# Kernel optimization log

Hardware: AMD Instinct MI355X
Metric: run time of the kernel (lower is better)

## Reference

```python
import jax, jax.numpy as jnp
import numpy as np

# dims: B batch, T timesteps, V nodes, D in-features, C channels, d pos-emb dim,
# TS = t_size (spatio-temporal window), P prediction steps, L layers (=4, fixed by GLU(C*4))
B, T, V, D, C, d, TS, P, L = 4, 12, 512, 1, 64, 8, 3, 12, 4
BETA = TS - 1


def setup_inputs() -> dict:
    key = jax.random.key(0)
    ks = jax.random.split(key, 30)
    n = lambda i, shape, s=1.0: jax.random.normal(ks[i], shape, dtype=jnp.float32) * s
    return dict(
        x=n(0, (B, T, V, D)),
        sape=n(1, (V, d)),
        tape=n(2, (B, T, 1, d)),
        srpe=n(3, (V, V, d)),
        trpe=n(4, (TS, 1, d)),
        zeros_x=jnp.zeros((B, BETA, V, C), jnp.float32),
        zeros_tape=jnp.zeros((B, BETA, 1, d), jnp.float32),
        range_mask=(jax.random.uniform(ks[5], (B, V, TS * V)) < 0.5).astype(jnp.float32),
        Wi=n(6, (D, C), D ** -0.5), bi=n(7, (C,), 0.02),
        gc_mu=n(8, (L, 6, d)), gc_sig=n(9, (L, 6, d), 0.5),
        Wg=n(10, (L, C, 2 * C), C ** -0.5), bg=n(11, (L, 2 * C), 0.02),
        Wsp=n(12, (L, d, 2 * C), d ** -0.5), Wtp=n(13, (L, d, 2 * C), d ** -0.5),
        fs_w=n(14, (L, C, C, T), (C * T) ** -0.5), fs_b=n(15, (L, C), 0.02),
        glu1_w=n(16, (L, 2 * C, C), C ** -0.5), glu1_b=n(17, (L, 2 * C), 0.02),
        gout_w=n(18, (8 * C, 4 * C), (4 * C) ** -0.5), gout_b=n(19, (8 * C,), 0.02),
        out_w=n(20, (P, 4 * C), (4 * C) ** -0.5), out_b=n(21, (P,), 0.02),
    )


def _glu_cv(w, b, y):
    # 1x1-conv GLU over channel dim of y: (B, Cin, V) -> (B, Cin, V)
    z = jnp.einsum('oc,bcv->bov', w, y) + b[None, :, None]
    zl, zr = jnp.split(z, 2, axis=1)
    return zl * jax.nn.sigmoid(zr)


def _forward(x, sape, tape, srpe, trpe, Wi, bi, gc_mu, gc_sig, Wg, bg, Wsp, Wtp,
             fs_w, fs_b, glu1_w, glu1_b, gout_w, gout_b, out_w, out_b,
             zeros_x, zeros_tape, range_mask):
    b_, t_ = x.shape[0], x.shape[1]
    v_ = sape.shape[0]
    ts = trpe.shape[0]
    widx = jnp.arange(t_)[:, None] + jnp.arange(ts)  # (T, t_size) sliding-window indices
    h = x @ Wi + bi                                   # InputLayer: B,T,V,C
    tape_pad = jnp.concatenate([zeros_tape, tape], axis=1)  # B,T+beta,1,d
    skips = []
    for l in range(gc_mu.shape[0]):
        mu, sig = gc_mu[l], gc_sig[l]
        gc = lambda emb, i: jnp.sum(-0.5 * (emb - mu[i]) ** 2 * sig[i] ** 2, axis=-1)
        # STPRI: Gaussian position-aware relation inference
        base = gc(sape, 0)[:, None] + gc(sape, 1)[None, :] + gc(srpe, 4)        # (V_i, V_j)
        per_t = gc(tape, 2)[:, :, 0][:, :, None] \
              + gc(tape_pad, 3)[:, :, 0][:, widx] \
              + gc(trpe, 5)[:, 0]                                               # B,T,t_size
        S = jnp.exp(per_t[:, :, :, None, None] + base)                          # B,T,k,i,j (<=1, safe)
        S = S.transpose(0, 1, 4, 2, 3).reshape(b_, t_, v_, ts * v_)             # B,T,j,(k*V+i)
        S = S * range_mask[:, None]                                             # masked relations
        # STPGConv: masked graph conv over the t_size*V window + gating
        x_pad = jnp.concatenate([zeros_x, h], axis=1)                           # B,T+beta,V,C
        xw = x_pad[:, widx].reshape(b_, t_, ts * v_, -1)                        # B,T,t_size*V,C
        g = jnp.einsum('btjm,btmc->btjc', S, xw) @ Wg[l] + bg[l]                # B,T,V,2C
        g = g + sape @ Wsp[l] + tape @ Wtp[l]                                   # +SE(V,2C) +TE(B,T,1,2C)
        gl, gr = jnp.split(g, 2, axis=-1)
        h = gl * jax.nn.sigmoid(gr)                                             # B,T,V,C
        # GFS: conv over time (kernel (1,T)) + GLU -> B,C,V
        y = jnp.einsum('bcvt,oct->bov', h.transpose(0, 3, 2, 1), fs_w[l]) + fs_b[l][None, :, None]
        skips.append(_glu_cv(glu1_w[l], glu1_b[l], y))
    s = _glu_cv(gout_w, gout_b, jnp.concatenate(skips, axis=1))                  # B,4C,V
    return jnp.einsum('oc,bcv->bov', out_w, s) + out_b[None, :, None]            # B,P,V


def reference(x, sape, tape, srpe, trpe, zeros_x, zeros_tape, range_mask, Wi, bi,
              gc_mu, gc_sig, Wg, bg, Wsp, Wtp, fs_w, fs_b, glu1_w, glu1_b,
              gout_w, gout_b, out_w, out_b):
    return _forward(x, sape, tape, srpe, trpe, Wi, bi, gc_mu, gc_sig, Wg, bg, Wsp, Wtp,
                    fs_w, fs_b, glu1_w, glu1_b, gout_w, gout_b, out_w, out_b,
                    zeros_x, zeros_tape, range_mask)
```

## Files before the change

kernel.cpp:

```cpp
#include <hip/hip_runtime.h>
#include <math.h>


typedef unsigned short u16;
typedef __attribute__((ext_vector_type(8))) short short8;
typedef __attribute__((ext_vector_type(4))) float f32x4;
typedef __attribute__((ext_vector_type(8))) unsigned short u16x8;
typedef __attribute__((ext_vector_type(4))) unsigned short u16x4;

#define MFMA16(a, b, c) __builtin_amdgcn_mfma_f32_16x16x32_bf16((a), (b), (c), 0, 0, 0)

__device__ __forceinline__ float b2f(u16 u) {
  union { unsigned int i; float f; } x; x.i = ((unsigned int)u) << 16; return x.f;
}
__device__ __forceinline__ u16 f2b(float f) {
  union { float f; unsigned int i; } x; x.f = f;
  unsigned int r = x.i + 0x7FFFu + ((x.i >> 16) & 1u);
  return (u16)(r >> 16);
}
__device__ __forceinline__ void ld8f(const float* __restrict__ p, float* f) {
  f32x4 a = *(const f32x4*)p;
  f32x4 b = *(const f32x4*)(p + 4);
  #pragma unroll
  for (int i = 0; i < 4; ++i) { f[i] = a[i]; f[4 + i] = b[i]; }
}
__device__ __forceinline__ float gcf(const float* e, const float* __restrict__ mu,
                                     const float* __restrict__ sg) {
  float s = 0.f;
  #pragma unroll
  for (int i = 0; i < 8; ++i) {
    float dm = e[i] - mu[i];
    s += dm * dm * sg[i] * sg[i];
  }
  return -0.5f * s;
}
__device__ __forceinline__ float sigm(float v) { return 1.0f / (1.0f + expf(-v)); }

__global__ __launch_bounds__(256) void prep_kernel(
    const float* __restrict__ x, const float* __restrict__ sape,
    const float* __restrict__ tape, const float* __restrict__ srpe,
    const float* __restrict__ trpe, const float* __restrict__ Wi,
    const float* __restrict__ bi, const float* __restrict__ gmu,
    const float* __restrict__ gsg, const float* __restrict__ Wg,
    const float* __restrict__ bg, const float* __restrict__ Wsp,
    const float* __restrict__ Wtp, const float* __restrict__ fsw,
    const float* __restrict__ mask,
    const float* __restrict__ g1w, const float* __restrict__ gw,
    const float* __restrict__ ow,
    u16* __restrict__ hT0, u16* __restrict__ Abf,
    float* __restrict__ spb, float* __restrict__ tpb,
    u16* __restrict__ fswT, u16* __restrict__ WgT, float* __restrict__ ev,
    u16* __restrict__ g1wB, u16* __restrict__ gwB, u16* __restrict__ owB) {
  const int tid = threadIdx.x;
  int bid = blockIdx.x;

  if (bid < 768) {
    int gid = bid * 256 + tid;
    int i8 = gid & 63, c = (gid >> 6) & 63, bt = gid >> 12;
    float xv[8];
    ld8f(&x[bt * 512 + i8 * 8], xv);
    float wic = Wi[c], bic = bi[c];
    u16x8 hv;
    #pragma unroll
    for (int ii = 0; ii < 8; ++ii) hv[ii] = f2b(xv[ii] * wic + bic);
    *(u16x8*)&hT0[gid * 8] = hv;
    return;
  }
  bid -= 768;
  if (bid < 1024) {
    int gid = bid * 256 + tid;
    int i = gid & 511, j = gid >> 9;
    float fi[8], fj[8], fr[8];
    ld8f(sape + i * 8, fi);
    ld8f(sape + j * 8, fj);
    ld8f(srpe + ((size_t)i * 512 + j) * 8, fr);
    u16 eb[4];
    #pragma unroll
    for (int l = 0; l < 4; ++l) {
      const float* mub = gmu + l * 48;
      const float* sgb = gsg + l * 48;
      float s = gcf(fi, mub + 0, sgb + 0)
              + gcf(fj, mub + 8, sgb + 8)
              + gcf(fr, mub + 32, sgb + 32);
      eb[l] = f2b(expf(s));
    }
    #pragma unroll
    for (int b = 0; b < 4; ++b)
      #pragma unroll
      for (int k = 0; k < 3; ++k) {
        float mv = mask[((size_t)(b * 512 + j)) * 1536 + k * 512 + i];
        u16 m = (mv != 0.f) ? (u16)0xFFFFu : (u16)0;
        #pragma unroll
        for (int l = 0; l < 4; ++l)
          Abf[((size_t)((l * 4 + b) * 512 + j)) * 1536 + k * 512 + i] = eb[l] & m;
      }
    return;
  }
  bid -= 1024;
  if (bid < 1024) {
    int gid = bid * 256 + tid;
    int o = gid & 127, j = (gid >> 7) & 511, l = gid >> 16;
    float a = 0.f;
    #pragma unroll
    for (int dd = 0; dd < 8; ++dd)
      a += sape[j * 8 + dd] * Wsp[(l * 8 + dd) * 128 + o];
    spb[gid] = a;
    return;
  }
  bid -= 1024;
  if (bid < 96) {
    int gid = bid * 256 + tid;
    int o = gid & 127, bt = (gid >> 7) % 48, l = gid / 6144;
    float a = bg[l * 128 + o];
    #pragma unroll
    for (int dd = 0; dd < 8; ++dd)
      a += tape[bt * 8 + dd] * Wtp[(l * 8 + dd) * 128 + o];
    tpb[gid] = a;
    return;
  }
  bid -= 96;
  if (bid < 768) {
    int gid = bid * 256 + tid;
    int kidx = gid % 768, rest = gid / 768;
    int o = rest & 63, l = rest >> 6;
    int c = kidx & 63, tt = kidx >> 6;
    fswT[gid] = f2b(fsw[((l * 64 + o) * 64 + c) * 12 + tt]);
    return;
  }
  bid -= 768;
  if (bid < 128) {
    int gid = bid * 256 + tid;
    int c = gid & 63, o = (gid >> 6) & 127, l = gid >> 13;
    WgT[gid] = f2b(Wg[(l * 64 + c) * 128 + o]);
    return;
  }
  bid -= 128;
  if (bid < 3) {
    int gid = bid * 256 + tid;
    if (gid < 576) {
      int k = gid % 3, t = (gid / 3) % 12, b = (gid / 36) % 4, l = gid / 144;
      const float* mub = gmu + l * 48;
      const float* sgb = gsg + l * 48;
      float e2[8], e3[8], e5[8];
      ld8f(tape + (b * 12 + t) * 8, e2);
      int tp = t + k - 2;
      if (tp >= 0) ld8f(tape + (b * 12 + tp) * 8, e3);
      else {
        #pragma unroll
        for (int ii = 0; ii < 8; ++ii) e3[ii] = 0.f;
      }
      ld8f(trpe + k * 8, e5);
      float s = gcf(e2, mub + 16, sgb + 16)
              + gcf(e3, mub + 24, sgb + 24)
              + gcf(e5, mub + 40, sgb + 40);
      ev[gid] = expf(s);
    }
    return;
  }
  bid -= 3;
  if (bid < 128) {
    int gid = bid * 256 + tid;
    g1wB[gid] = f2b(g1w[gid]);
    return;
  }
  bid -= 128;
  if (bid < 512) {
    int gid = bid * 256 + tid;
    gwB[gid] = f2b(gw[gid]);
    return;
  }
  bid -= 512;
  {
    int gid = bid * 256 + tid;
    if (gid < 3072) owB[gid] = f2b(ow[gid]);
  }
}

__global__ __launch_bounds__(256) void agg_kernel(
    const u16* __restrict__ Abfl, const u16* __restrict__ hT,
    u16* __restrict__ G) {
  __shared__ u16 As[128][72];
  __shared__ u16 Bs[128][72];
  const int tid = threadIdx.x, wid = tid >> 6, lane = tid & 63;
  const int l16 = lane & 15, quad = lane >> 4;
  const int bid = blockIdx.x;
  const int nt = bid % 6;
  const int mt = (bid / 6) & 3;
  const int k  = (bid / 24) % 3;
  const int b  = bid / 72;
  const int wm = wid >> 1, wn = wid & 1;

  const u16* Arow0 = Abfl + ((size_t)(b * 512 + mt * 128)) * 1536 + k * 512;
  f32x4 acc[4][4] = {};

  for (int it = 0; it < 8; ++it) {
    const int i0 = it * 64;
    #pragma unroll
    for (int s = 0; s < 4; ++s) {
      int idx = s * 256 + tid;
      int r = idx >> 3, ch = (idx & 7) * 8;
      *(u16x8*)&As[r][ch] = *(const u16x8*)&Arow0[(size_t)r * 1536 + i0 + ch];
      int tp = nt * 2 + (r >> 6), c = r & 63;
      *(u16x8*)&Bs[r][ch] =
          *(const u16x8*)&hT[((size_t)((b * 12 + tp) * 64 + c)) * 512 + i0 + ch];
    }
    __syncthreads();
    #pragma unroll
    for (int ks = 0; ks < 2; ++ks) {
      short8 af[4], bf[4];
      #pragma unroll
      for (int mb = 0; mb < 4; ++mb)
        af[mb] = *(const short8*)&As[wm * 64 + mb * 16 + l16][ks * 32 + quad * 8];
      #pragma unroll
      for (int nb = 0; nb < 4; ++nb)
        bf[nb] = *(const short8*)&Bs[wn * 64 + nb * 16 + l16][ks * 32 + quad * 8];
      #pragma unroll
      for (int mb = 0; mb < 4; ++mb)
        #pragma unroll
        for (int nb = 0; nb < 4; ++nb)
          acc[mb][nb] = MFMA16(af[mb], bf[nb], acc[mb][nb]);
    }
    __syncthreads();
  }

  u16* base = &As[0][0];
  #pragma unroll
  for (int mb = 0; mb < 4; ++mb)
    #pragma unroll
    for (int nb = 0; nb < 4; ++nb) {
      int n = wn * 64 + nb * 16 + l16;
      #pragma unroll
      for (int r = 0; r < 4; ++r) {
        int m = wm * 64 + mb * 16 + quad * 4 + r;
        base[m * 128 + n] = f2b(acc[mb][nb][r]);
      }
    }
  __syncthreads();
  u16* Gp = G + ((size_t)((b * 3 + k) * 512 + mt * 128)) * 768 + nt * 128;
  #pragma unroll
  for (int s = 0; s < 8; ++s) {
    int idx = s * 256 + tid;
    int m = idx >> 4, ch = (idx & 15) * 8;
    *(u16x8*)&Gp[(size_t)m * 768 + ch] = *(const u16x8*)&base[m * 128 + ch];
  }
}

__global__ __launch_bounds__(256) void combine_kernel(
    const u16* __restrict__ G, const float* __restrict__ evl,
    const u16* __restrict__ WgTl, const float* __restrict__ spbl,
    const float* __restrict__ tpbl, const u16* __restrict__ fswTl,
    u16* __restrict__ hTout, float* __restrict__ yptl) {
  __shared__ u16 aggL[128][72];
  __shared__ u16 hL[128][72];
  const int tid = threadIdx.x, wid = tid >> 6, lane = tid & 63;
  const int l16 = lane & 15, quad = lane >> 4;
  const int bid = blockIdx.x;
  const int mt = bid & 3;
  const int bt = bid >> 2;
  const int b = bt / 12, t = bt - b * 12;

  {
    int j = tid >> 1;
    int c0 = (tid & 1) * 32;
    float accv[32];
    #pragma unroll
    for (int ii = 0; ii < 32; ++ii) accv[ii] = 0.f;
    #pragma unroll
    for (int k = 0; k < 3; ++k) {
      int tp = t + k - 2;
      if (tp < 0) continue;
      float ek = evl[bt * 3 + k];
      const u16* gp = &G[((size_t)((b * 3 + k) * 512 + mt * 128 + j)) * 768 + tp * 64 + c0];
      #pragma unroll
      for (int s = 0; s < 4; ++s) {
        u16x8 gv = *(const u16x8*)&gp[s * 8];
        #pragma unroll
        for (int ii = 0; ii < 8; ++ii) accv[s * 8 + ii] += b2f(gv[ii]) * ek;
      }
    }
    #pragma unroll
    for (int s = 0; s < 4; ++s) {
      u16x8 ov;
      #pragma unroll
      for (int ii = 0; ii < 8; ++ii) ov[ii] = f2b(accv[s * 8 + ii]);
      *(u16x8*)&aggL[j][c0 + s * 8] = ov;
    }
  }
  __syncthreads();

  f32x4 acc2[8][2] = {};
  #pragma unroll
  for (int ks = 0; ks < 2; ++ks) {
    short8 bf[2];
    #pragma unroll
    for (int nb = 0; nb < 2; ++nb)
      bf[nb] = *(const short8*)&aggL[wid * 32 + nb * 16 + l16][ks * 32 + quad * 8];
    #pragma unroll
    for (int mb = 0; mb < 8; ++mb) {
      short8 a = *(const short8*)&WgTl[(mb * 16 + l16) * 64 + ks * 32 + quad * 8];
      acc2[mb][0] = MFMA16(a, bf[0], acc2[mb][0]);
      acc2[mb][1] = MFMA16(a, bf[1], acc2[mb][1]);
    }
  }

  #pragma unroll
  for (int mb = 0; mb < 4; ++mb) {
    int ob = mb * 16 + quad * 4;
    #pragma unroll
    for (int nb = 0; nb < 2; ++nb) {
      int jl = wid * 32 + nb * 16 + l16;
      int jg = mt * 128 + jl;
      f32x4 spl = *(const f32x4*)&spbl[jg * 128 + ob];
      f32x4 spr = *(const f32x4*)&spbl[jg * 128 + 64 + ob];
      f32x4 tpl = *(const f32x4*)&tpbl[bt * 128 + ob];
      f32x4 tpr = *(const f32x4*)&tpbl[bt * 128 + 64 + ob];
      #pragma unroll
      for (int r = 0; r < 4; ++r) {
        float vl = acc2[mb][nb][r] + spl[r] + tpl[r];
        float vr = acc2[mb + 4][nb][r] + spr[r] + tpr[r];
        u16 hb = f2b(vl * sigm(vr));
        hTout[((size_t)((b * 12 + t) * 64 + ob + r)) * 512 + jg] = hb;
        hL[jl][ob + r] = hb;
      }
    }
  }
  __syncthreads();

  f32x4 accY[4][2] = {};
  #pragma unroll
  for (int ks = 0; ks < 2; ++ks) {
    short8 bfv[2];
    #pragma unroll
    for (int nb = 0; nb < 2; ++nb)
      bfv[nb] = *(const short8*)&hL[wid * 32 + nb * 16 + l16][ks * 32 + quad * 8];
    #pragma unroll
    for (int mb = 0; mb < 4; ++mb) {
      short8 a = *(const short8*)&fswTl[(mb * 16 + l16) * 768 + t * 64 + ks * 32 + quad * 8];
      accY[mb][0] = MFMA16(a, bfv[0], accY[mb][0]);
      accY[mb][1] = MFMA16(a, bfv[1], accY[mb][1]);
    }
  }
  #pragma unroll
  for (int mb = 0; mb < 4; ++mb)
    #pragma unroll
    for (int nb = 0; nb < 2; ++nb) {
      int j = mt * 128 + wid * 32 + nb * 16 + l16;
      #pragma unroll
      for (int r = 0; r < 4; ++r) {
        int o = mb * 16 + quad * 4 + r;
        yptl[((size_t)(bt * 64 + o)) * 512 + j] = accY[mb][nb][r];
      }
    }
}

__global__ __launch_bounds__(256) void reduce_kernel(
    const float* __restrict__ ypt, const float* __restrict__ fsb,
    u16* __restrict__ yB) {
  int gid = blockIdx.x * 256 + threadIdx.x;
  int j4 = gid & 127, o = (gid >> 7) & 63, b = (gid >> 13) & 3, l = gid >> 15;
  const float* base = &ypt[(size_t)l * 1572864 +
                           ((size_t)((b * 12) * 64 + o)) * 512 + j4 * 4];
  float fb = fsb[l * 64 + o];
  f32x4 s = {fb, fb, fb, fb};
  #pragma unroll
  for (int t = 0; t < 12; ++t) s += *(const f32x4*)&base[(size_t)t * 32768];
  u16x4 pk;
  #pragma unroll
  for (int ii = 0; ii < 4; ++ii) pk[ii] = f2b(s[ii]);
  *(u16x4*)&yB[((size_t)((l * 4 + b) * 64 + o)) * 512 + j4 * 4] = pk;
}

__global__ __launch_bounds__(256) void glu1cat_kernel(
    const u16* __restrict__ yB, const u16* __restrict__ g1wB,
    const float* __restrict__ g1b, u16* __restrict__ catB) {
  __shared__ u16 yL[128][72];
  const int tid = threadIdx.x, wid = tid >> 6, lane = tid & 63;
  const int l16 = lane & 15, quad = lane >> 4;
  const int l = blockIdx.x >> 4;
  const int b = (blockIdx.x >> 2) & 3;
  const int v0 = (blockIdx.x & 3) * 128;

  {
    int o = tid & 63, sv = tid >> 6;
    const u16* src = &yB[((size_t)((l * 4 + b) * 64 + o)) * 512 + v0 + sv * 32];
    u16x8 p0 = *(const u16x8*)&src[0];
    u16x8 p1 = *(const u16x8*)&src[8];
    u16x8 p2 = *(const u16x8*)&src[16];
    u16x8 p3 = *(const u16x8*)&src[24];
    #pragma unroll
    for (int ii = 0; ii < 8; ++ii) {
      yL[sv * 32 + ii][o] = p0[ii];
      yL[sv * 32 + 8 + ii][o] = p1[ii];
      yL[sv * 32 + 16 + ii][o] = p2[ii];
      yL[sv * 32 + 24 + ii][o] = p3[ii];
    }
  }
  __syncthreads();

  f32x4 acc[2][8] = {};
  #pragma unroll
  for (int ks = 0; ks < 2; ++ks) {
    short8 a0 = *(const short8*)&g1wB[l * 8192 + (wid * 16 + l16) * 64 +
                                      ks * 32 + quad * 8];
    short8 a1 = *(const short8*)&g1wB[l * 8192 + (64 + wid * 16 + l16) * 64 +
                                      ks * 32 + quad * 8];
    #pragma unroll
    for (int nb = 0; nb < 8; ++nb) {
      short8 bf = *(const short8*)&yL[nb * 16 + l16][ks * 32 + quad * 8];
      acc[0][nb] = MFMA16(a0, bf, acc[0][nb]);
      acc[1][nb] = MFMA16(a1, bf, acc[1][nb]);
    }
  }
  #pragma unroll
  for (int nb = 0; nb < 8; ++nb) {
    int v = v0 + nb * 16 + l16;
    int oc = wid * 16 + quad * 4;
    u16x4 pk;
    #pragma unroll
    for (int r = 0; r < 4; ++r) {
      float zl = acc[0][nb][r] + g1b[l * 128 + oc + r];
      float zr = acc[1][nb][r] + g1b[l * 128 + 64 + oc + r];
      pk[r] = f2b(zl * sigm(zr));
    }
    *(u16x4*)&catB[((size_t)(b * 512 + v)) * 256 + l * 64 + oc] = pk;
  }
}

__global__ __launch_bounds__(256) void gout_kernel(
    const u16* __restrict__ catB, const u16* __restrict__ gwB,
    const float* __restrict__ gb, u16* __restrict__ sB) {
  __shared__ u16 cL[64][264];
  const int tid = threadIdx.x, wid = tid >> 6, lane = tid & 63;
  const int l16 = lane & 15, quad = lane >> 4;
  const int wm = wid >> 1, wn = wid & 1;
  const int b = blockIdx.x >> 6;
  const int v0 = ((blockIdx.x >> 3) & 7) * 64;
  const int cc0 = (blockIdx.x & 7) * 32;

  {
    int v = tid >> 2, seg = (tid & 3) * 64;
    const u16* src = &catB[((size_t)(b * 512 + v0 + v)) * 256 + seg];
    #pragma unroll
    for (int s = 0; s < 8; ++s)
      *(u16x8*)&cL[v][seg + s * 8] = *(const u16x8*)&src[s * 8];
  }
  __syncthreads();

  f32x4 acc[2][2] = {};
  #pragma unroll
  for (int ks = 0; ks < 8; ++ks) {
    short8 aL = *(const short8*)&gwB[(cc0 + wm * 16 + l16) * 256 +
                                     ks * 32 + quad * 8];
    short8 aH = *(const short8*)&gwB[(256 + cc0 + wm * 16 + l16) * 256 +
                                     ks * 32 + quad * 8];
    #pragma unroll
    for (int nb = 0; nb < 2; ++nb) {
      short8 bf = *(const short8*)&cL[wn * 32 + nb * 16 + l16][ks * 32 + quad * 8];
      acc[0][nb] = MFMA16(aL, bf, acc[0][nb]);
      acc[1][nb] = MFMA16(aH, bf, acc[1][nb]);
    }
  }
  #pragma unroll
  for (int nb = 0; nb < 2; ++nb) {
    int v = v0 + wn * 32 + nb * 16 + l16;
    int cc = cc0 + wm * 16 + quad * 4;
    u16x4 pk;
    #pragma unroll
    for (int r = 0; r < 4; ++r) {
      float zl = acc[0][nb][r] + gb[cc + r];
      float zr = acc[1][nb][r] + gb[256 + cc + r];
      pk[r] = f2b(zl * sigm(zr));
    }
    *(u16x4*)&sB[((size_t)(b * 512 + v)) * 256 + cc] = pk;
  }
}

__global__ __launch_bounds__(256) void head_kernel(
    const u16* __restrict__ sB, const u16* __restrict__ owB,
    const float* __restrict__ obv, float* __restrict__ out) {
  const int tid = threadIdx.x, wid = tid >> 6, lane = tid & 63;
  const int l16 = lane & 15, quad = lane >> 4;
  const int b = blockIdx.x >> 3;
  const int v0 = (blockIdx.x & 7) * 64;

  f32x4 acc = {};
  #pragma unroll
  for (int ks = 0; ks < 8; ++ks) {
    short8 a;
    if (l16 < 12) a = *(const short8*)&owB[l16 * 256 + ks * 32 + quad * 8];
    else {
      #pragma unroll
      for (int ii = 0; ii < 8; ++ii) a[ii] = 0;
    }
    short8 bf = *(const short8*)&sB[((size_t)(b * 512 + v0 + wid * 16 + l16)) * 256 +
                                    ks * 32 + quad * 8];
    acc = MFMA16(a, bf, acc);
  }
  #pragma unroll
  for (int r = 0; r < 4; ++r) {
    int p = quad * 4 + r;
    if (p < 12)
      out[(b * 12 + p) * 512 + v0 + wid * 16 + l16] = acc[r] + obv[p];
  }
}

extern "C" void kernel_launch(void* const* d_in, const int* in_sizes, int n_in,
                              void* d_out, int out_size, void* d_ws, size_t ws_size,
                              hipStream_t stream) {
  const float* x    = (const float*)d_in[0];
  const float* sape = (const float*)d_in[1];
  const float* tape = (const float*)d_in[2];
  const float* srpe = (const float*)d_in[3];
  const float* trpe = (const float*)d_in[4];
  const float* mask = (const float*)d_in[7];
  const float* Wi   = (const float*)d_in[8];
  const float* bi   = (const float*)d_in[9];
  const float* gmu  = (const float*)d_in[10];
  const float* gsg  = (const float*)d_in[11];
  const float* Wg   = (const float*)d_in[12];
  const float* bg   = (const float*)d_in[13];
  const float* Wsp  = (const float*)d_in[14];
  const float* Wtp  = (const float*)d_in[15];
  const float* fsw  = (const float*)d_in[16];
  const float* fsb  = (const float*)d_in[17];
  const float* g1w  = (const float*)d_in[18];
  const float* g1b  = (const float*)d_in[19];
  const float* gow  = (const float*)d_in[20];
  const float* gob  = (const float*)d_in[21];
  const float* ow   = (const float*)d_in[22];
  const float* obv  = (const float*)d_in[23];

  char* w = (char*)d_ws;
  u16*   hT_a = (u16*)(w + 0);
  u16*   hT_b = (u16*)(w + 3145728);
  u16*   Abf  = (u16*)(w + 6291456);
  u16*   G    = (u16*)(w + 31457280);
  u16*   fswT = (u16*)(w + 40894464);
  u16*   WgT  = (u16*)(w + 41287680);
  u16*   g1wB = (u16*)(w + 41353216);
  u16*   gwB  = (u16*)(w + 41418752);
  u16*   owB  = (u16*)(w + 41680896);
  float* spb  = (float*)(w + 41689088);
  float* tpb  = (float*)(w + 42737664);
  float* ev   = (float*)(w + 42835968);
  float* ypt  = (float*)(w + 42852352);
  u16*   yB   = (u16*)(w + 68018176);
  u16*   catB = (u16*)(w + 70115328);
  u16*   sB   = (u16*)(w + 71163904);

  prep_kernel<<<4463, 256, 0, stream>>>(x, sape, tape, srpe, trpe, Wi, bi, gmu, gsg,
                                        Wg, bg, Wsp, Wtp, fsw, mask, g1w, gow, ow,
                                        hT_a, Abf, spb, tpb, fswT, WgT, ev,
                                        g1wB, gwB, owB);
  u16* hin = hT_a;
  u16* hout = hT_b;
  for (int l = 0; l < 4; ++l) {
    agg_kernel<<<288, 256, 0, stream>>>(Abf + (size_t)l * 3145728, hin, G);
    combine_kernel<<<192, 256, 0, stream>>>(G, ev + l * 144, WgT + l * 8192,
                                            spb + l * 65536, tpb + l * 6144,
                                            fswT + l * 49152, hout,
                                            ypt + (size_t)l * 1572864);
    u16* tmp = hin; hin = hout; hout = tmp;
  }
  reduce_kernel<<<512, 256, 0, stream>>>(ypt, fsb, yB);
  glu1cat_kernel<<<64, 256, 0, stream>>>(yB, g1wB, g1b, catB);
  gout_kernel<<<256, 256, 0, stream>>>(catB, gwB, gob, sB);
  head_kernel<<<32, 256, 0, stream>>>(sB, owB, obv, (float*)d_out);
}
```

Before: 247.6 us.

## Fuse all stages into one persistent kernel with grid-wide barriers

Replaces the sequence of thirteen kernel launches with a single persistent kernel of 256 blocks. Each block loops over the original block indices of every stage, and stages are separated by software grid barriers built from atomic counters. This removes launch overhead and the inter-kernel gaps. In exchange it adds barrier spin cost, needs a memset of the counters each call, and relies on all 256 blocks being co-resident. Stages with more than 256 jobs, such as prep and agg, now run in multiple waves.

```diff
diff --git a/kernel.cpp b/kernel.cpp
--- a/kernel.cpp
+++ b/kernel.cpp
@@ -36,34 +36,39 @@
 }
 __device__ __forceinline__ float sigm(float v) { return 1.0f / (1.0f + expf(-v)); }
 
-__global__ __launch_bounds__(256) void prep_kernel(
-    const float* __restrict__ x, const float* __restrict__ sape,
-    const float* __restrict__ tape, const float* __restrict__ srpe,
-    const float* __restrict__ trpe, const float* __restrict__ Wi,
-    const float* __restrict__ bi, const float* __restrict__ gmu,
-    const float* __restrict__ gsg, const float* __restrict__ Wg,
-    const float* __restrict__ bg, const float* __restrict__ Wsp,
-    const float* __restrict__ Wtp, const float* __restrict__ fsw,
-    const float* __restrict__ mask,
-    const float* __restrict__ g1w, const float* __restrict__ gw,
-    const float* __restrict__ ow,
-    u16* __restrict__ hT0, u16* __restrict__ Abf,
-    float* __restrict__ spb, float* __restrict__ tpb,
-    u16* __restrict__ fswT, u16* __restrict__ WgT, float* __restrict__ ev,
-    u16* __restrict__ g1wB, u16* __restrict__ gwB, u16* __restrict__ owB) {
+__device__ __forceinline__ void gsync(int* bar) {
+  __syncthreads();
+  if (threadIdx.x == 0) {
+    __threadfence();
+    atomicAdd(bar, 1);
+    while (atomicAdd(bar, 0) < 256) __builtin_amdgcn_s_sleep(8);
+    __threadfence();
+  }
+  __syncthreads();
+}
+
+struct MegaArgs {
+  const float *x, *sape, *tape, *srpe, *trpe, *Wi, *bi, *gmu, *gsg, *Wg, *bg,
+              *Wsp, *Wtp, *fsw, *mask, *g1w, *gw, *ow, *fsb, *g1b, *gob, *obv;
+  u16 *hT_a, *hT_b, *Abf, *G, *fswT, *WgT, *g1wB, *gwB, *owB, *yB, *catB, *sB;
+  float *spb, *tpb, *ev, *ypt;
+  float *outp;
+  int *bars;
+};
+
+__device__ void prep_body(const MegaArgs& a, int bid) {
   const int tid = threadIdx.x;
-  int bid = blockIdx.x;
 
   if (bid < 768) {
     int gid = bid * 256 + tid;
     int i8 = gid & 63, c = (gid >> 6) & 63, bt = gid >> 12;
     float xv[8];
-    ld8f(&x[bt * 512 + i8 * 8], xv);
-    float wic = Wi[c], bic = bi[c];
+    ld8f(&a.x[bt * 512 + i8 * 8], xv);
+    float wic = a.Wi[c], bic = a.bi[c];
     u16x8 hv;
     #pragma unroll
     for (int ii = 0; ii < 8; ++ii) hv[ii] = f2b(xv[ii] * wic + bic);
-    *(u16x8*)&hT0[gid * 8] = hv;
+    *(u16x8*)&a.hT_a[gid * 8] = hv;
     return;
   }
   bid -= 768;
@@ -71,14 +76,14 @@
     int gid = bid * 256 + tid;
     int i = gid & 511, j = gid >> 9;
     float fi[8], fj[8], fr[8];
-    ld8f(sape + i * 8, fi);
-    ld8f(sape + j * 8, fj);
-    ld8f(srpe + ((size_t)i * 512 + j) * 8, fr);
+    ld8f(a.sape + i * 8, fi);
+    ld8f(a.sape + j * 8, fj);
+    ld8f(a.srpe + ((size_t)i * 512 + j) * 8, fr);
     u16 eb[4];
     #pragma unroll
     for (int l = 0; l < 4; ++l) {
-      const float* mub = gmu + l * 48;
-      const float* sgb = gsg + l * 48;
+      const float* mub = a.gmu + l * 48;
+      const float* sgb = a.gsg + l * 48;
       float s = gcf(fi, mub + 0, sgb + 0)
               + gcf(fj, mub + 8, sgb + 8)
               + gcf(fr, mub + 32, sgb + 32);
@@ -88,11 +93,11 @@
     for (int b = 0; b < 4; ++b)
       #pragma unroll
       for (int k = 0; k < 3; ++k) {
-        float mv = mask[((size_t)(b * 512 + j)) * 1536 + k * 512 + i];
+        float mv = a.mask[((size_t)(b * 512 + j)) * 1536 + k * 512 + i];
         u16 m = (mv != 0.f) ? (u16)0xFFFFu : (u16)0;
         #pragma unroll
         for (int l = 0; l < 4; ++l)
-          Abf[((size_t)((l * 4 + b) * 512 + j)) * 1536 + k * 512 + i] = eb[l] & m;
+          a.Abf[((size_t)((l * 4 + b) * 512 + j)) * 1536 + k * 512 + i] = eb[l] & m;
       }
     return;
   }
@@ -100,22 +105,22 @@
   if (bid < 1024) {
     int gid = bid * 256 + tid;
     int o = gid & 127, j = (gid >> 7) & 511, l = gid >> 16;
-    float a = 0.f;
+    float s = 0.f;
     #pragma unroll
     for (int dd = 0; dd < 8; ++dd)
-      a += sape[j * 8 + dd] * Wsp[(l * 8 + dd) * 128 + o];
-    spb[gid] = a;
+      s += a.sape[j * 8 + dd] * a.Wsp[(l * 8 + dd) * 128 + o];
+    a.spb[gid] = s;
     return;
   }
   bid -= 1024;
   if (bid < 96) {
     int gid = bid * 256 + tid;
     int o = gid & 127, bt = (gid >> 7) % 48, l = gid / 6144;
-    float a = bg[l * 128 + o];
+    float s = a.bg[l * 128 + o];
     #pragma unroll
     for (int dd = 0; dd < 8; ++dd)
-      a += tape[bt * 8 + dd] * Wtp[(l * 8 + dd) * 128 + o];
-    tpb[gid] = a;
+      s += a.tape[bt * 8 + dd] * a.Wtp[(l * 8 + dd) * 128 + o];
+    a.tpb[gid] = s;
     return;
   }
   bid -= 96;
@@ -124,14 +129,14 @@
     int kidx = gid % 768, rest = gid / 768;
     int o = rest & 63, l = rest >> 6;
     int c = kidx & 63, tt = kidx >> 6;
-    fswT[gid] = f2b(fsw[((l * 64 + o) * 64 + c) * 12 + tt]);
+    a.fswT[gid] = f2b(a.fsw[((l * 64 + o) * 64 + c) * 12 + tt]);
     return;
   }
   bid -= 768;
   if (bid < 128) {
     int gid = bid * 256 + tid;
     int c = gid & 63, o = (gid >> 6) & 127, l = gid >> 13;
-    WgT[gid] = f2b(Wg[(l * 64 + c) * 128 + o]);
+    a.WgT[gid] = f2b(a.Wg[(l * 64 + c) * 128 + o]);
     return;
   }
   bid -= 128;
@@ -139,51 +144,38 @@
     int gid = bid * 256 + tid;
     if (gid < 576) {
       int k = gid % 3, t = (gid / 3) % 12, b = (gid / 36) % 4, l = gid / 144;
-      const float* mub = gmu + l * 48;
-      const float* sgb = gsg + l * 48;
+      const float* mub = a.gmu + l * 48;
+      const float* sgb = a.gsg + l * 48;
       float e2[8], e3[8], e5[8];
-      ld8f(tape + (b * 12 + t) * 8, e2);
+      ld8f(a.tape + (b * 12 + t) * 8, e2);
       int tp = t + k - 2;
-      if (tp >= 0) ld8f(tape + (b * 12 + tp) * 8, e3);
+      if (tp >= 0) ld8f(a.tape + (b * 12 + tp) * 8, e3);
       else {
         #pragma unroll
         for (int ii = 0; ii < 8; ++ii) e3[ii] = 0.f;
       }
-      ld8f(trpe + k * 8, e5);
+      ld8f(a.trpe + k * 8, e5);
       float s = gcf(e2, mub + 16, sgb + 16)
               + gcf(e3, mub + 24, sgb + 24)
               + gcf(e5, mub + 40, sgb + 40);
-      ev[gid] = expf(s);
+      a.ev[gid] = expf(s);
     }
     return;
   }
   bid -= 3;
-  if (bid < 128) {
-    int gid = bid * 256 + tid;
-    g1wB[gid] = f2b(g1w[gid]);
-    return;
-  }
+  if (bid < 128) { int gid = bid * 256 + tid; a.g1wB[gid] = f2b(a.g1w[gid]); return; }
   bid -= 128;
-  if (bid < 512) {
-    int gid = bid * 256 + tid;
-    gwB[gid] = f2b(gw[gid]);
-    return;
-  }
+  if (bid < 512) { int gid = bid * 256 + tid; a.gwB[gid] = f2b(a.gw[gid]); return; }
   bid -= 512;
-  {
-    int gid = bid * 256 + tid;
-    if (gid < 3072) owB[gid] = f2b(ow[gid]);
-  }
-}
-
-__global__ __launch_bounds__(256) void agg_kernel(
-    const u16* __restrict__ Abfl, const u16* __restrict__ hT,
-    u16* __restrict__ G) {
-  __shared__ u16 As[128][72];
-  __shared__ u16 Bs[128][72];
+  { int gid = bid * 256 + tid; if (gid < 3072) a.owB[gid] = f2b(a.ow[gid]); }
+}
+
+__device__ void agg_body(const MegaArgs& a, int bid, const u16* __restrict__ Abfl,
+                         const u16* __restrict__ hT, char* smem) {
+  u16 (*As)[72] = (u16 (*)[72])smem;
+  u16 (*Bs)[72] = (u16 (*)[72])(smem + 18432);
   const int tid = threadIdx.x, wid = tid >> 6, lane = tid & 63;
   const int l16 = lane & 15, quad = lane >> 4;
-  const int bid = blockIdx.x;
   const int nt = bid % 6;
   const int mt = (bid / 6) & 3;
   const int k  = (bid / 24) % 3;
@@ -223,7 +215,7 @@
     __syncthreads();
   }
 
-  u16* base = &As[0][0];
+  u16* base = (u16*)smem;
   #pragma unroll
   for (int mb = 0; mb < 4; ++mb)
     #pragma unroll
@@ -236,25 +228,29 @@
       }
     }
   __syncthreads();
-  u16* Gp = G + ((size_t)((b * 3 + k) * 512 + mt * 128)) * 768 + nt * 128;
+  u16* Gp = a.G + ((size_t)((b * 3 + k) * 512 + mt * 128)) * 768 + nt * 128;
   #pragma unroll
   for (int s = 0; s < 8; ++s) {
     int idx = s * 256 + tid;
     int m = idx >> 4, ch = (idx & 15) * 8;
     *(u16x8*)&Gp[(size_t)m * 768 + ch] = *(const u16x8*)&base[m * 128 + ch];
   }
-}
-
-__global__ __launch_bounds__(256) void combine_kernel(
-    const u16* __restrict__ G, const float* __restrict__ evl,
-    const u16* __restrict__ WgTl, const float* __restrict__ spbl,
-    const float* __restrict__ tpbl, const u16* __restrict__ fswTl,
-    u16* __restrict__ hTout, float* __restrict__ yptl) {
-  __shared__ u16 aggL[128][72];
-  __shared__ u16 hL[128][72];
+  __syncthreads();
+}
+
+__device__ void combine_body(const MegaArgs& a, int bid, int l,
+                             u16* __restrict__ hTout, char* smem) {
+  u16 (*aggL)[72] = (u16 (*)[72])smem;
+  u16 (*hL)[72]   = (u16 (*)[72])(smem + 18432);
+  const float* evl  = a.ev  + l * 144;
+  const u16*   WgTl = a.WgT + l * 8192;
+  const float* spbl = a.spb + l * 65536;
+  const float* tpbl = a.tpb + l * 6144;
+  const u16*   fswTl = a.fswT + l * 49152;
+  float* yptl = a.ypt + (size_t)l * 1572864;
+
   const int tid = threadIdx.x, wid = tid >> 6, lane = tid & 63;
   const int l16 = lane & 15, quad = lane >> 4;
-  const int bid = blockIdx.x;
   const int mt = bid & 3;
   const int bt = bid >> 2;
   const int b = bt / 12, t = bt - b * 12;
@@ -270,7 +266,7 @@
       int tp = t + k - 2;
       if (tp < 0) continue;
       float ek = evl[bt * 3 + k];
-      const u16* gp = &G[((size_t)((b * 3 + k) * 512 + mt * 128 + j)) * 768 + tp * 64 + c0];
+      const u16* gp = &a.G[((size_t)((b * 3 + k) * 512 + mt * 128 + j)) * 768 + tp * 64 + c0];
       #pragma unroll
       for (int s = 0; s < 4; ++s) {
         u16x8 gv = *(const u16x8*)&gp[s * 8];
@@ -297,9 +293,9 @@
       bf[nb] = *(const short8*)&aggL[wid * 32 + nb * 16 + l16][ks * 32 + quad * 8];
     #pragma unroll
     for (int mb = 0; mb < 8; ++mb) {
-      short8 a = *(const short8*)&WgTl[(mb * 16 + l16) * 64 + ks * 32 + quad * 8];
-      acc2[mb][0] = MFMA16(a, bf[0], acc2[mb][0]);
-      acc2[mb][1] = MFMA16(a, bf[1], acc2[mb][1]);
+      short8 aa = *(const short8*)&WgTl[(mb * 16 + l16) * 64 + ks * 32 + quad * 8];
+      acc2[mb][0] = MFMA16(aa, bf[0], acc2[mb][0]);
+      acc2[mb][1] = MFMA16(aa, bf[1], acc2[mb][1]);
     }
   }
 
@@ -335,9 +331,9 @@
       bfv[nb] = *(const short8*)&hL[wid * 32 + nb * 16 + l16][ks * 32 + quad * 8];
     #pragma unroll
     for (int mb = 0; mb < 4; ++mb) {
-      short8 a = *(const short8*)&fswTl[(mb * 16 + l16) * 768 + t * 64 + ks * 32 + quad * 8];
-      accY[mb][0] = MFMA16(a, bfv[0], accY[mb][0]);
-      accY[mb][1] = MFMA16(a, bfv[1], accY[mb][1]);
+      short8 aa = *(const short8*)&fswTl[(mb * 16 + l16) * 768 + t * 64 + ks * 32 + quad * 8];
+      accY[mb][0] = MFMA16(aa, bfv[0], accY[mb][0]);
+      accY[mb][1] = MFMA16(aa, bfv[1], accY[mb][1]);
     }
   }
   #pragma unroll
@@ -351,38 +347,35 @@
         yptl[((size_t)(bt * 64 + o)) * 512 + j] = accY[mb][nb][r];
       }
     }
-}
-
-__global__ __launch_bounds__(256) void reduce_kernel(
-    const float* __restrict__ ypt, const float* __restrict__ fsb,
-    u16* __restrict__ yB) {
-  int gid = blockIdx.x * 256 + threadIdx.x;
+  __syncthreads();
+}
+
+__device__ void reduce_body(const MegaArgs& a, int bid) {
+  int gid = bid * 256 + threadIdx.x;
   int j4 = gid & 127, o = (gid >> 7) & 63, b = (gid >> 13) & 3, l = gid >> 15;
-  const float* base = &ypt[(size_t)l * 1572864 +
-                           ((size_t)((b * 12) * 64 + o)) * 512 + j4 * 4];
-  float fb = fsb[l * 64 + o];
+  const float* base = &a.ypt[(size_t)l * 1572864 +
+                             ((size_t)((b * 12) * 64 + o)) * 512 + j4 * 4];
+  float fb = a.fsb[l * 64 + o];
   f32x4 s = {fb, fb, fb, fb};
   #pragma unroll
   for (int t = 0; t < 12; ++t) s += *(const f32x4*)&base[(size_t)t * 32768];
   u16x4 pk;
   #pragma unroll
   for (int ii = 0; ii < 4; ++ii) pk[ii] = f2b(s[ii]);
-  *(u16x4*)&yB[((size_t)((l * 4 + b) * 64 + o)) * 512 + j4 * 4] = pk;
-}
-
-__global__ __launch_bounds__(256) void glu1cat_kernel(
-    const u16* __restrict__ yB, const u16* __restrict__ g1wB,
-    const float* __restrict__ g1b, u16* __restrict__ catB) {
-  __shared__ u16 yL[128][72];
+  *(u16x4*)&a.yB[((size_t)((l * 4 + b) * 64 + o)) * 512 + j4 * 4] = pk;
+}
+
+__device__ void glu1cat_body(const MegaArgs& a, int bid, char* smem) {
+  u16 (*yL)[72] = (u16 (*)[72])smem;
   const int tid = threadIdx.x, wid = tid >> 6, lane = tid & 63;
   const int l16 = lane & 15, quad = lane >> 4;
-  const int l = blockIdx.x >> 4;
-  const int b = (blockIdx.x >> 2) & 3;
-  const int v0 = (blockIdx.x & 3) * 128;
+  const int l = bid >> 4;
+  const int b = (bid >> 2) & 3;
+  const int v0 = (bid & 3) * 128;
 
   {
     int o = tid & 63, sv = tid >> 6;
-    const u16* src = &yB[((size_t)((l * 4 + b) * 64 + o)) * 512 + v0 + sv * 32];
+    const u16* src = &a.yB[((size_t)((l * 4 + b) * 64 + o)) * 512 + v0 + sv * 32];
     u16x8 p0 = *(const u16x8*)&src[0];
     u16x8 p1 = *(const u16x8*)&src[8];
     u16x8 p2 = *(const u16x8*)&src[16];
@@ -400,10 +393,10 @@
   f32x4 acc[2][8] = {};
   #pragma unroll
   for (int ks = 0; ks < 2; ++ks) {
-    short8 a0 = *(const short8*)&g1wB[l * 8192 + (wid * 16 + l16) * 64 +
-                                      ks * 32 + quad * 8];
-    short8 a1 = *(const short8*)&g1wB[l * 8192 + (64 + wid * 16 + l16) * 64 +
-                                      ks * 32 + quad * 8];
+    short8 a0 = *(const short8*)&a.g1wB[l * 8192 + (wid * 16 + l16) * 64 +
+                                        ks * 32 + quad * 8];
+    short8 a1 = *(const short8*)&a.g1wB[l * 8192 + (64 + wid * 16 + l16) * 64 +
+                                        ks * 32 + quad * 8];
     #pragma unroll
     for (int nb = 0; nb < 8; ++nb) {
       short8 bf = *(const short8*)&yL[nb * 16 + l16][ks * 32 + quad * 8];
@@ -418,28 +411,27 @@
     u16x4 pk;
     #pragma unroll
     for (int r = 0; r < 4; ++r) {
-      float zl = acc[0][nb][r] + g1b[l * 128 + oc + r];
-      float zr = acc[1][nb][r] + g1b[l * 128 + 64 + oc + r];
+      float zl = acc[0][nb][r] + a.g1b[l * 128 + oc + r];
+      float zr = acc[1][nb][r] + a.g1b[l * 128 + 64 + oc + r];
       pk[r] = f2b(zl * sigm(zr));
     }
-    *(u16x4*)&catB[((size_t)(b * 512 + v)) * 256 + l * 64 + oc] = pk;
-  }
-}
-
-__global__ __launch_bounds__(256) void gout_kernel(
-    const u16* __restrict__ catB, const u16* __restrict__ gwB,
-    const float* __restrict__ gb, u16* __restrict__ sB) {
-  __shared__ u16 cL[64][264];
+    *(u16x4*)&a.catB[((size_t)(b * 512 + v)) * 256 + l * 64 + oc] = pk;
+  }
+  __syncthreads();
+}
+
+__device__ void gout_body(const MegaArgs& a, int bid, char* smem) {
+  u16 (*cL)[264] = (u16 (*)[264])smem;
   const int tid = threadIdx.x, wid = tid >> 6, lane = tid & 63;
   const int l16 = lane & 15, quad = lane >> 4;
   const int wm = wid >> 1, wn = wid & 1;
-  const int b = blockIdx.x >> 6;
-  const int v0 = ((blockIdx.x >> 3) & 7) * 64;
-  const int cc0 = (blockIdx.x & 7) * 32;
+  const int b = bid >> 6;
+  const int v0 = ((bid >> 3) & 7) * 64;
+  const int cc0 = (bid & 7) * 32;
 
   {
     int v = tid >> 2, seg = (tid & 3) * 64;
-    const u16* src = &catB[((size_t)(b * 512 + v0 + v)) * 256 + seg];
+    const u16* src = &a.catB[((size_t)(b * 512 + v0 + v)) * 256 + seg];
     #pragma unroll
     for (int s = 0; s < 8; ++s)
       *(u16x8*)&cL[v][seg + s * 8] = *(const u16x8*)&src[s * 8];
@@ -449,10 +441,10 @@
   f32x4 acc[2][2] = {};
   #pragma unroll
   for (int ks = 0; ks < 8; ++ks) {
-    short8 aL = *(const short8*)&gwB[(cc0 + wm * 16 + l16) * 256 +
-                                     ks * 32 + quad * 8];
-    short8 aH = *(const short8*)&gwB[(256 + cc0 + wm * 16 + l16) * 256 +
-                                     ks * 32 + quad * 8];
+    short8 aL = *(const short8*)&a.gwB[(cc0 + wm * 16 + l16) * 256 +
+                                       ks * 32 + quad * 8];
+    short8 aH = *(const short8*)&a.gwB[(256 + cc0 + wm * 16 + l16) * 256 +
+                                       ks * 32 + quad * 8];
     #pragma unroll
     for (int nb = 0; nb < 2; ++nb) {
       short8 bf = *(const short8*)&cL[wn * 32 + nb * 16 + l16][ks * 32 + quad * 8];
@@ -467,103 +459,116 @@
     u16x4 pk;
     #pragma unroll
     for (int r = 0; r < 4; ++r) {
-      float zl = acc[0][nb][r] + gb[cc + r];
-      float zr = acc[1][nb][r] + gb[256 + cc + r];
+      float zl = acc[0][nb][r] + a.gob[cc + r];
+      float zr = acc[1][nb][r] + a.gob[256 + cc + r];
       pk[r] = f2b(zl * sigm(zr));
     }
-    *(u16x4*)&sB[((size_t)(b * 512 + v)) * 256 + cc] = pk;
-  }
-}
-
-__global__ __launch_bounds__(256) void head_kernel(
-    const u16* __restrict__ sB, const u16* __restrict__ owB,
-    const float* __restrict__ obv, float* __restrict__ out) {
+    *(u16x4*)&a.sB[((size_t)(b * 512 + v)) * 256 + cc] = pk;
+  }
+  __syncthreads();
+}
+
+__device__ void head_body(const MegaArgs& a, int bid) {
   const int tid = threadIdx.x, wid = tid >> 6, lane = tid & 63;
   const int l16 = lane & 15, quad = lane >> 4;
-  const int b = blockIdx.x >> 3;
-  const int v0 = (blockIdx.x & 7) * 64;
+  const int b = bid >> 3;
+  const int v0 = (bid & 7) * 64;
 
   f32x4 acc = {};
   #pragma unroll
   for (int ks = 0; ks < 8; ++ks) {
-    short8 a;
-    if (l16 < 12) a = *(const short8*)&owB[l16 * 256 + ks * 32 + quad * 8];
+    short8 aa;
+    if (l16 < 12) aa = *(const short8*)&a.owB[l16 * 256 + ks * 32 + quad * 8];
     else {
       #pragma unroll
-      for (int ii = 0; ii < 8; ++ii) a[ii] = 0;
-    }
-    short8 bf = *(const short8*)&sB[((size_t)(b * 512 + v0 + wid * 16 + l16)) * 256 +
-                                    ks * 32 + quad * 8];
-    acc = MFMA16(a, bf, acc);
+      for (int ii = 0; ii < 8; ++ii) aa[ii] = 0;
+    }
+    short8 bf = *(const short8*)&a.sB[((size_t)(b * 512 + v0 + wid * 16 + l16)) * 256 +
+                                      ks * 32 + quad * 8];
+    acc = MFMA16(aa, bf, acc);
   }
   #pragma unroll
   for (int r = 0; r < 4; ++r) {
     int p = quad * 4 + r;
     if (p < 12)
-      out[(b * 12 + p) * 512 + v0 + wid * 16 + l16] = acc[r] + obv[p];
-  }
+      a.outp[(b * 12 + p) * 512 + v0 + wid * 16 + l16] = acc[r] + a.obv[p];
+  }
+}
+
+__global__ __launch_bounds__(256, 1) void mega_kernel(MegaArgs a) {
+  __shared__ __align__(16) char smem[36864];
+
+  for (int job = blockIdx.x; job < 4463; job += 256) prep_body(a, job);
+  gsync(&a.bars[0]);
+
+  for (int l = 0; l < 4; ++l) {
+    const u16* hin = (l & 1) ? a.hT_b : a.hT_a;
+    u16* hout = (l & 1) ? a.hT_a : a.hT_b;
+    const u16* Abfl = a.Abf + (size_t)l * 3145728;
+    for (int job = blockIdx.x; job < 288; job += 256)
+      agg_body(a, job, Abfl, hin, smem);
+    gsync(&a.bars[1 + 2 * l]);
+    for (int job = blockIdx.x; job < 192; job += 256)
+      combine_body(a, job, l, hout, smem);
+    gsync(&a.bars[2 + 2 * l]);
+  }
+
+  for (int job = blockIdx.x; job < 512; job += 256) reduce_body(a, job);
+  gsync(&a.bars[9]);
+  for (int job = blockIdx.x; job < 64; job += 256) glu1cat_body(a, job, smem);
+  gsync(&a.bars[10]);
+  for (int job = blockIdx.x; job < 256; job += 256) gout_body(a, job, smem);
+  gsync(&a.bars[11]);
+  for (int job = blockIdx.x; job < 32; job += 256) head_body(a, job);
 }
 
 extern "C" void kernel_launch(void* const* d_in, const int* in_sizes, int n_in,
                               void* d_out, int out_size, void* d_ws, size_t ws_size,
                               hipStream_t stream) {
-  const float* x    = (const float*)d_in[0];
-  const float* sape = (const float*)d_in[1];
-  const float* tape = (const float*)d_in[2];
-  const float* srpe = (const float*)d_in[3];
-  const float* trpe = (const float*)d_in[4];
-  const float* mask = (const float*)d_in[7];
-  const float* Wi   = (const float*)d_in[8];
-  const float* bi   = (const float*)d_in[9];
-  const float* gmu  = (const float*)d_in[10];
-  const float* gsg  = (const float*)d_in[11];
-  const float* Wg   = (const float*)d_in[12];
-  const float* bg   = (const float*)d_in[13];
-  const float* Wsp  = (const float*)d_in[14];
-  const float* Wtp  = (const float*)d_in[15];
-  const float* fsw  = (const float*)d_in[16];
-  const float* fsb  = (const float*)d_in[17];
-  const float* g1w  = (const float*)d_in[18];
-  const float* g1b  = (const float*)d_in[19];
-  const float* gow  = (const float*)d_in[20];
-  const float* gob  = (const float*)d_in[21];
-  const float* ow   = (const float*)d_in[22];
-  const float* obv  = (const float*)d_in[23];
-
   char* w = (char*)d_ws;
-  u16*   hT_a = (u16*)(w + 0);
-  u16*   hT_b = (u16*)(w + 3145728);
-  u16*   Abf  = (u16*)(w + 6291456);
-  u16*   G    = (u16*)(w + 31457280);
-  u16*   fswT = (u16*)(w + 40894464);
-  u16*   WgT  = (u16*)(w + 41287680);
-  u16*   g1wB = (u16*)(w + 41353216);
-  u16*   gwB  = (u16*)(w + 41418752);
-  u16*   owB  = (u16*)(w + 41680896);
-  float* spb  = (float*)(w + 41689088);
-  float* tpb  = (float*)(w + 42737664);
-  float* ev   = (float*)(w + 42835968);
-  float* ypt  = (float*)(w + 42852352);
-  u16*   yB   = (u16*)(w + 68018176);
-  u16*   catB = (u16*)(w + 70115328);
-  u16*   sB   = (u16*)(w + 71163904);
-
-  prep_kernel<<<4463, 256, 0, stream>>>(x, sape, tape, srpe, trpe, Wi, bi, gmu, gsg,
-                                        Wg, bg, Wsp, Wtp, fsw, mask, g1w, gow, ow,
-                                        hT_a, Abf, spb, tpb, fswT, WgT, ev,
-                                        g1wB, gwB, owB);
-  u16* hin = hT_a;
-  u16* hout = hT_b;
-  for (int l = 0; l < 4; ++l) {
-    agg_kernel<<<288, 256, 0, stream>>>(Abf + (size_t)l * 3145728, hin, G);
-    combine_kernel<<<192, 256, 0, stream>>>(G, ev + l * 144, WgT + l * 8192,
-                                            spb + l * 65536, tpb + l * 6144,
-                                            fswT + l * 49152, hout,
-                                            ypt + (size_t)l * 1572864);
-    u16* tmp = hin; hin = hout; hout = tmp;
-  }
-  reduce_kernel<<<512, 256, 0, stream>>>(ypt, fsb, yB);
-  glu1cat_kernel<<<64, 256, 0, stream>>>(yB, g1wB, g1b, catB);
-  gout_kernel<<<256, 256, 0, stream>>>(catB, gwB, gob, sB);
-  head_kernel<<<32, 256, 0, stream>>>(sB, owB, obv, (float*)d_out);
-}
+  MegaArgs a;
+  a.x    = (const float*)d_in[0];
+  a.sape = (const float*)d_in[1];
+  a.tape = (const float*)d_in[2];
+  a.srpe = (const float*)d_in[3];
+  a.trpe = (const float*)d_in[4];
+  a.mask = (const float*)d_in[7];
+  a.Wi   = (const float*)d_in[8];
+  a.bi   = (const float*)d_in[9];
+  a.gmu  = (const float*)d_in[10];
+  a.gsg  = (const float*)d_in[11];
+  a.Wg   = (const float*)d_in[12];
+  a.bg   = (const float*)d_in[13];
+  a.Wsp  = (const float*)d_in[14];
+  a.Wtp  = (const float*)d_in[15];
+  a.fsw  = (const float*)d_in[16];
+  a.fsb  = (const float*)d_in[17];
+  a.g1w  = (const float*)d_in[18];
+  a.g1b  = (const float*)d_in[19];
+  a.gw   = (const float*)d_in[20];
+  a.gob  = (const float*)d_in[21];
+  a.ow   = (const float*)d_in[22];
+  a.obv  = (const float*)d_in[23];
+
+  a.hT_a = (u16*)(w + 0);
+  a.hT_b = (u16*)(w + 3145728);
+  a.Abf  = (u16*)(w + 6291456);
+  a.G    = (u16*)(w + 31457280);
+  a.fswT = (u16*)(w + 40894464);
+  a.WgT  = (u16*)(w + 41287680);
+  a.g1wB = (u16*)(w + 41353216);
+  a.gwB  = (u16*)(w + 41418752);
+  a.owB  = (u16*)(w + 41680896);
+  a.spb  = (float*)(w + 41689088);
+  a.tpb  = (float*)(w + 42737664);
+  a.ev   = (float*)(w + 42835968);
+  a.ypt  = (float*)(w + 42852352);
+  a.yB   = (u16*)(w + 68018176);
+  a.catB = (u16*)(w + 70115328);
+  a.sB   = (u16*)(w + 71163904);
+  a.bars = (int*)(w + 72212480);
+  a.outp = (float*)d_out;
+
+  hipMemsetAsync(a.bars, 0, 128, stream);
+  mega_kernel<<<256, 256, 0, stream>>>(a);
+}
```

Result: slower. 526.8 us (+112.7%).

## Replace materialized masked adjacency with bitmask plus shared exp table, split-K agg

Applied to the files above, without the earlier changes.

Instead of writing a full bf16 masked adjacency tensor per layer and batch (about 25MB), prep now stores one bf16 exp table per layer plus a packed bit mask built with ballot. The agg kernel rebuilds the masked A tile on the fly from the table and mask bytes. It also splits the K dimension in half to double the grid, writing two partial G buffers that combine sums. This cuts memory traffic and raises parallelism, at the cost of extra G traffic in combine and per-element select work in agg.

```diff
diff --git a/kernel.cpp b/kernel.cpp
--- a/kernel.cpp
+++ b/kernel.cpp
@@ -3,12 +3,15 @@
 
 
 typedef unsigned short u16;
+typedef unsigned char u8;
+typedef unsigned long long u64;
 typedef __attribute__((ext_vector_type(8))) short short8;
 typedef __attribute__((ext_vector_type(4))) float f32x4;
 typedef __attribute__((ext_vector_type(8))) unsigned short u16x8;
 typedef __attribute__((ext_vector_type(4))) unsigned short u16x4;
 
 #define MFMA16(a, b, c) __builtin_amdgcn_mfma_f32_16x16x32_bf16((a), (b), (c), 0, 0, 0)
+#define GHALF 9437184
 
 __device__ __forceinline__ float b2f(u16 u) {
   union { unsigned int i; float f; } x; x.i = ((unsigned int)u) << 16; return x.f;
@@ -47,7 +50,7 @@
     const float* __restrict__ mask,
     const float* __restrict__ g1w, const float* __restrict__ gw,
     const float* __restrict__ ow,
-    u16* __restrict__ hT0, u16* __restrict__ Abf,
+    u16* __restrict__ hT0, u16* __restrict__ expbT, u64* __restrict__ mbits,
     float* __restrict__ spb, float* __restrict__ tpb,
     u16* __restrict__ fswT, u16* __restrict__ WgT, float* __restrict__ ev,
     u16* __restrict__ g1wB, u16* __restrict__ gwB, u16* __restrict__ owB) {
@@ -74,7 +77,6 @@
     ld8f(sape + i * 8, fi);
     ld8f(sape + j * 8, fj);
     ld8f(srpe + ((size_t)i * 512 + j) * 8, fr);
-    u16 eb[4];
     #pragma unroll
     for (int l = 0; l < 4; ++l) {
       const float* mub = gmu + l * 48;
@@ -82,17 +84,16 @@
       float s = gcf(fi, mub + 0, sgb + 0)
               + gcf(fj, mub + 8, sgb + 8)
               + gcf(fr, mub + 32, sgb + 32);
-      eb[l] = f2b(expf(s));
+      expbT[l * 262144 + j * 512 + i] = f2b(expf(s));
     }
     #pragma unroll
     for (int b = 0; b < 4; ++b)
       #pragma unroll
       for (int k = 0; k < 3; ++k) {
         float mv = mask[((size_t)(b * 512 + j)) * 1536 + k * 512 + i];
-        u16 m = (mv != 0.f) ? (u16)0xFFFFu : (u16)0;
-        #pragma unroll
-        for (int l = 0; l < 4; ++l)
-          Abf[((size_t)((l * 4 + b) * 512 + j)) * 1536 + k * 512 + i] = eb[l] & m;
+        u64 bal = __ballot(mv != 0.f);
+        if ((tid & 63) == 0)
+          mbits[((size_t)((b * 512 + j) * 3 + k)) * 8 + (i >> 6)] = bal;
       }
     return;
   }
@@ -100,22 +101,22 @@
   if (bid < 1024) {
     int gid = bid * 256 + tid;
     int o = gid & 127, j = (gid >> 7) & 511, l = gid >> 16;
-    float a = 0.f;
+    float s = 0.f;
     #pragma unroll
     for (int dd = 0; dd < 8; ++dd)
-      a += sape[j * 8 + dd] * Wsp[(l * 8 + dd) * 128 + o];
-    spb[gid] = a;
+      s += sape[j * 8 + dd] * Wsp[(l * 8 + dd) * 128 + o];
+    spb[gid] = s;
     return;
   }
   bid -= 1024;
   if (bid < 96) {
     int gid = bid * 256 + tid;
     int o = gid & 127, bt = (gid >> 7) % 48, l = gid / 6144;
-    float a = bg[l * 128 + o];
+    float s = bg[l * 128 + o];
     #pragma unroll
     for (int dd = 0; dd < 8; ++dd)
-      a += tape[bt * 8 + dd] * Wtp[(l * 8 + dd) * 128 + o];
-    tpb[gid] = a;
+      s += tape[bt * 8 + dd] * Wtp[(l * 8 + dd) * 128 + o];
+    tpb[gid] = s;
     return;
   }
   bid -= 96;
@@ -177,8 +178,8 @@
 }
 
 __global__ __launch_bounds__(256) void agg_kernel(
-    const u16* __restrict__ Abfl, const u16* __restrict__ hT,
-    u16* __restrict__ G) {
+    const u16* __restrict__ ebl, const u8* __restrict__ mbytes,
+    const u16* __restrict__ hT, u16* __restrict__ G) {
   __shared__ u16 As[128][72];
   __shared__ u16 Bs[128][72];
   const int tid = threadIdx.x, wid = tid >> 6, lane = tid & 63;
@@ -187,19 +188,25 @@
   const int nt = bid % 6;
   const int mt = (bid / 6) & 3;
   const int k  = (bid / 24) % 3;
-  const int b  = bid / 72;
+  const int half = (bid / 72) & 1;
+  const int b  = bid / 144;
   const int wm = wid >> 1, wn = wid & 1;
 
-  const u16* Arow0 = Abfl + ((size_t)(b * 512 + mt * 128)) * 1536 + k * 512;
   f32x4 acc[4][4] = {};
 
-  for (int it = 0; it < 8; ++it) {
-    const int i0 = it * 64;
+  for (int it = 0; it < 4; ++it) {
+    const int i0 = half * 256 + it * 64;
     #pragma unroll
     for (int s = 0; s < 4; ++s) {
       int idx = s * 256 + tid;
       int r = idx >> 3, ch = (idx & 7) * 8;
-      *(u16x8*)&As[r][ch] = *(const u16x8*)&Arow0[(size_t)r * 1536 + i0 + ch];
+      u16x8 ev = *(const u16x8*)&ebl[(size_t)(mt * 128 + r) * 512 + i0 + ch];
+      u8 mby = mbytes[((size_t)((b * 512 + mt * 128 + r) * 3 + k)) * 64 +
+                      ((i0 + ch) >> 3)];
+      u16x8 av;
+      #pragma unroll
+      for (int ii = 0; ii < 8; ++ii) av[ii] = ((mby >> ii) & 1) ? ev[ii] : (u16)0;
+      *(u16x8*)&As[r][ch] = av;
       int tp = nt * 2 + (r >> 6), c = r & 63;
       *(u16x8*)&Bs[r][ch] =
           *(const u16x8*)&hT[((size_t)((b * 12 + tp) * 64 + c)) * 512 + i0 + ch];
@@ -236,7 +243,8 @@
       }
     }
   __syncthreads();
-  u16* Gp = G + ((size_t)((b * 3 + k) * 512 + mt * 128)) * 768 + nt * 128;
+  u16* Gp = G + (size_t)half * GHALF +
+            ((size_t)((b * 3 + k) * 512 + mt * 128)) * 768 + nt * 128;
   #pragma unroll
   for (int s = 0; s < 8; ++s) {
     int idx = s * 256 + tid;
@@ -270,12 +278,15 @@
       int tp = t + k - 2;
       if (tp < 0) continue;
       float ek = evl[bt * 3 + k];
-      const u16* gp = &G[((size_t)((b * 3 + k) * 512 + mt * 128 + j)) * 768 + tp * 64 + c0];
+      const u16* gp0 = &G[((size_t)((b * 3 + k) * 512 + mt * 128 + j)) * 768 + tp * 64 + c0];
+      const u16* gp1 = gp0 + (size_t)GHALF;
       #pragma unroll
       for (int s = 0; s < 4; ++s) {
-        u16x8 gv = *(const u16x8*)&gp[s * 8];
+        u16x8 g0 = *(const u16x8*)&gp0[s * 8];
+        u16x8 g1 = *(const u16x8*)&gp1[s * 8];
         #pragma unroll
-        for (int ii = 0; ii < 8; ++ii) accv[s * 8 + ii] += b2f(gv[ii]) * ek;
+        for (int ii = 0; ii < 8; ++ii)
+          accv[s * 8 + ii] += (b2f(g0[ii]) + b2f(g1[ii])) * ek;
       }
     }
     #pragma unroll
@@ -531,31 +542,33 @@
   const float* obv  = (const float*)d_in[23];
 
   char* w = (char*)d_ws;
-  u16*   hT_a = (u16*)(w + 0);
-  u16*   hT_b = (u16*)(w + 3145728);
-  u16*   Abf  = (u16*)(w + 6291456);
-  u16*   G    = (u16*)(w + 31457280);
-  u16*   fswT = (u16*)(w + 40894464);
-  u16*   WgT  = (u16*)(w + 41287680);
-  u16*   g1wB = (u16*)(w + 41353216);
-  u16*   gwB  = (u16*)(w + 41418752);
-  u16*   owB  = (u16*)(w + 41680896);
-  float* spb  = (float*)(w + 41689088);
-  float* tpb  = (float*)(w + 42737664);
-  float* ev   = (float*)(w + 42835968);
-  float* ypt  = (float*)(w + 42852352);
-  u16*   yB   = (u16*)(w + 68018176);
-  u16*   catB = (u16*)(w + 70115328);
-  u16*   sB   = (u16*)(w + 71163904);
+  u16*   hT_a  = (u16*)(w + 0);
+  u16*   hT_b  = (u16*)(w + 3145728);
+  u16*   expbT = (u16*)(w + 6291456);
+  u64*   mbits = (u64*)(w + 8388608);
+  u16*   G     = (u16*)(w + 8781824);
+  u16*   fswT  = (u16*)(w + 46530560);
+  u16*   WgT   = (u16*)(w + 46923776);
+  u16*   g1wB  = (u16*)(w + 46989312);
+  u16*   gwB   = (u16*)(w + 47054848);
+  u16*   owB   = (u16*)(w + 47316992);
+  float* spb   = (float*)(w + 47325184);
+  float* tpb   = (float*)(w + 48373760);
+  float* ev    = (float*)(w + 48472064);
+  float* ypt   = (float*)(w + 48488448);
+  u16*   yB    = (u16*)(w + 73654272);
+  u16*   catB  = (u16*)(w + 75751424);
+  u16*   sB    = (u16*)(w + 76800000);
 
   prep_kernel<<<4463, 256, 0, stream>>>(x, sape, tape, srpe, trpe, Wi, bi, gmu, gsg,
                                         Wg, bg, Wsp, Wtp, fsw, mask, g1w, gow, ow,
-                                        hT_a, Abf, spb, tpb, fswT, WgT, ev,
+                                        hT_a, expbT, mbits, spb, tpb, fswT, WgT, ev,
                                         g1wB, gwB, owB);
   u16* hin = hT_a;
   u16* hout = hT_b;
   for (int l = 0; l < 4; ++l) {
-    agg_kernel<<<288, 256, 0, stream>>>(Abf + (size_t)l * 3145728, hin, G);
+    agg_kernel<<<576, 256, 0, stream>>>(expbT + l * 262144, (const u8*)mbits,
+                                        hin, G);
     combine_kernel<<<192, 256, 0, stream>>>(G, ev + l * 144, WgT + l * 8192,
                                             spb + l * 65536, tpb + l * 6144,
                                             fswT + l * 49152, hout,
```

After: 263.2 us. +6.3%, slower.
